# Performance work log

Hardware: AMD Instinct MI355X
Metric: run time of the kernel (lower is better)

Reference implementation:

```python
import jax, jax.numpy as jnp
import numpy as np

D_MODEL = 1024
BLOCK_SIZE = 2048


def setup_inputs() -> dict:
    key = jax.random.key(0)
    ks = jax.random.split(key, 9)
    B, T, C = 4, 2048, D_MODEL
    s = 1.0 / np.sqrt(C)
    return {
        "x": jax.random.normal(ks[0], (B, T, C), dtype=jnp.float32),
        "Wq": jax.random.normal(ks[1], (C, C), dtype=jnp.float32) * s,
        "bq": jnp.zeros((C,), dtype=jnp.float32),
        "Wk": jax.random.normal(ks[2], (C, C), dtype=jnp.float32) * s,
        "bk": jnp.zeros((C,), dtype=jnp.float32),
        "Wv": jax.random.normal(ks[3], (C, C), dtype=jnp.float32) * s,
        "bv": jnp.zeros((C,), dtype=jnp.float32),
        "Wo": jax.random.normal(ks[4], (C, C), dtype=jnp.float32) * s,
        "bo": jnp.zeros((C,), dtype=jnp.float32),
    }


def reference(x, Wq, bq, Wk, bk, Wv, bv, Wo, bo):
    B, T, C = x.shape
    q = x @ Wq + bq
    k = x @ Wk + bk
    v = x @ Wv + bv
    # NOTE: original module never splits heads; attention is over full d_model
    score = jnp.einsum("btc,bsc->bts", q, k) / jnp.sqrt(jnp.asarray(C, x.dtype))
    causal = jnp.tril(jnp.ones((T, T), dtype=bool))
    score = jnp.where(causal, score, jnp.asarray(-jnp.inf, x.dtype))
    probs = jax.nn.softmax(score, axis=-1)
    out = jnp.einsum("bts,bsc->btc", probs, v)
    return out @ Wo + bo
```

## Files before the change

### kernel.cpp

```cpp
#include <hip/hip_runtime.h>
#include <hip/hip_bf16.h>
#include <stdint.h>


typedef __attribute__((ext_vector_type(8))) __bf16 bf16x8;
typedef __attribute__((ext_vector_type(4))) float f32x4;

#define MFMA16(A, B, C) __builtin_amdgcn_mfma_f32_16x16x32_bf16(A, B, C, 0, 0, 0)
#define BAR() asm volatile("s_barrier" ::: "memory")

#define T_SEQ 2048
#define D_MOD 1024

static __device__ __forceinline__ void gload_lds16(const void* g, void* l) {
  __builtin_amdgcn_global_load_lds(
      (const __attribute__((address_space(1))) void*)g,
      (__attribute__((address_space(3))) void*)l, 16, 0, 0);
}

__global__ void cvt_bf16_kernel(const float* __restrict__ in,
                                __bf16* __restrict__ out, int n8) {
  int i = blockIdx.x * blockDim.x + threadIdx.x;
  if (i < n8) {
    const float4* p = (const float4*)(in + (size_t)i * 8);
    float4 a = p[0], b = p[1];
    bf16x8 o;
    o[0] = (__bf16)a.x; o[1] = (__bf16)a.y; o[2] = (__bf16)a.z; o[3] = (__bf16)a.w;
    o[4] = (__bf16)b.x; o[5] = (__bf16)b.y; o[6] = (__bf16)b.z; o[7] = (__bf16)b.w;
    *(bf16x8*)(out + (size_t)i * 8) = o;
  }
}

__global__ void transpose_cvt_kernel(const float* __restrict__ W,
                                     __bf16* __restrict__ Wt) {
  __shared__ float tile[32][33];
  int tx = threadIdx.x, ty = threadIdx.y;
  int bx = blockIdx.x * 32, by = blockIdx.y * 32;
#pragma unroll
  for (int i = 0; i < 4; i++)
    tile[ty + 8 * i][tx] = W[(size_t)(by + ty + 8 * i) * D_MOD + bx + tx];
  __syncthreads();
#pragma unroll
  for (int i = 0; i < 4; i++)
    Wt[(size_t)(bx + ty + 8 * i) * D_MOD + by + tx] = (__bf16)tile[tx][ty + 8 * i];
}

__global__ void transpose_v_kernel(const __bf16* __restrict__ V,
                                   __bf16* __restrict__ Vt) {
  __shared__ __bf16 tile[32][33];
  int tx = threadIdx.x, ty = threadIdx.y;
  int b = blockIdx.z;
  int t0 = blockIdx.x * 32, d0 = blockIdx.y * 32;
  const __bf16* Vb = V + (size_t)b * T_SEQ * D_MOD;
  __bf16* Vtb = Vt + (size_t)b * D_MOD * T_SEQ;
#pragma unroll
  for (int i = 0; i < 4; i++)
    tile[ty + 8 * i][tx] = Vb[(size_t)(t0 + ty + 8 * i) * D_MOD + d0 + tx];
  __syncthreads();
#pragma unroll
  for (int i = 0; i < 4; i++)
    Vtb[(size_t)(d0 + ty + 8 * i) * T_SEQ + t0 + tx] = tile[tx][ty + 8 * i];
}

template <int MG, int NG>
static __device__ __forceinline__ void mfma_quad(f32x4 (&acc)[8][4],
                                                 const bf16x8 (&aR)[4][2],
                                                 const bf16x8 (&bR)[2][2]) {
#pragma unroll
  for (int i = 0; i < 4; i++)
#pragma unroll
    for (int n = 0; n < 2; n++)
#pragma unroll
      for (int kk = 0; kk < 2; kk++)
        acc[MG * 4 + i][NG * 2 + n] =
            MFMA16(aR[i][kk], bR[n][kk], acc[MG * 4 + i][NG * 2 + n]);
}

template <int MODE>
__global__ __launch_bounds__(512, 2) void gemm8_kernel(
    const __bf16* __restrict__ A, const __bf16* __restrict__ Bt,
    const float* __restrict__ b0, const float* __restrict__ b1,
    const float* __restrict__ b2, void* __restrict__ o0,
    void* __restrict__ o1, void* __restrict__ o2, int lda, int ldb,
    size_t bsA, size_t bsB, size_t bsC) {
  constexpr int NT = 16;
  __shared__ __align__(16) char lds[131072];
#define ABUF(p, h) (lds + ((p) * 2 + (h)) * 16384)
#define BBUF(p, h) (lds + 65536 + ((p) * 2 + (h)) * 16384)

  const int tid = threadIdx.x;
  const int w = tid >> 6, l = tid & 63;
  const int wr = w >> 2, wc = w & 3;
  int bm, bn;
  if (MODE == 0) {
    const int cpx = gridDim.x >> 3;
    const int swz = ((int)blockIdx.x & 7) * cpx + ((int)blockIdx.x >> 3);
    bm = (swz / 12) * 256;
    bn = (swz % 12) * 256;
  } else {
    if ((int)blockIdx.y > (int)blockIdx.x) return;
    bm = blockIdx.x * 256;
    bn = blockIdx.y * 256;
  }
  const int z = blockIdx.z;
  A += (size_t)z * bsA;
  Bt += (size_t)z * bsB;

  const int grow = l >> 2;
  const int cswz = (l & 3) ^ ((l >> 3) & 3);
  const int rlo = l & 15;
  const int xsw = (((l >> 4) ^ ((l >> 1) & 3)) << 4);

#define STAGE_A(t, h)                                                        \
  {                                                                          \
    const __bf16* g = A + (size_t)(bm + (h) * 128 + w * 16 + grow) * lda +   \
                      (t) * 64 + cswz * 8;                                   \
    char* d = ABUF((t) & 1, h) + w * 1024 + l * 16;                          \
    gload_lds16(g, d);                                                       \
    gload_lds16(g + 32, d + 8192);                                           \
  }
#define STAGE_B(t, h)                                                        \
  {                                                                          \
    const __bf16* g = Bt + (size_t)(bn + (h) * 128 + w * 16 + grow) * ldb +  \
                      (t) * 64 + cswz * 8;                                   \
    char* d = BBUF((t) & 1, h) + w * 1024 + l * 16;                          \
    gload_lds16(g, d);                                                       \
    gload_lds16(g + 32, d + 8192);                                           \
  }
#define LDA_FRAG(p, g, i, kk)                                     \
  (*(const bf16x8*)(ABUF(p, wr) + (kk) * 8192 +                   \
                    ((g) * 64 + (i) * 16 + rlo) * 64 + xsw))
#define LDB_FRAG(p, g, n, kk)                                     \
  (*(const bf16x8*)(BBUF(p, (wc >> 1)) + (kk) * 8192 +            \
                    ((wc & 1) * 64 + (g) * 32 + (n) * 16 + rlo) * 64 + xsw))

  f32x4 acc[8][4] = {};
  STAGE_A(0, 0); STAGE_A(0, 1);
  STAGE_B(0, 0); STAGE_B(0, 1);
  STAGE_A(1, 0); STAGE_A(1, 1);
  asm volatile("s_waitcnt vmcnt(4)" ::: "memory");
  BAR();

  for (int t = 0; t < NT; ++t) {
    const int p = t & 1;
    bf16x8 a[4][2], b[2][2];
#pragma unroll
    for (int i = 0; i < 4; i++) {
      a[i][0] = LDA_FRAG(p, 0, i, 0);
      a[i][1] = LDA_FRAG(p, 0, i, 1);
    }
#pragma unroll
    for (int n = 0; n < 2; n++) {
      b[n][0] = LDB_FRAG(p, 0, n, 0);
      b[n][1] = LDB_FRAG(p, 0, n, 1);
    }
    if (t + 1 < NT) STAGE_B(t + 1, 0);
    BAR();
    __builtin_amdgcn_s_setprio(1);
    mfma_quad<0, 0>(acc, a, b);
    __builtin_amdgcn_s_setprio(0);
    BAR();
    bf16x8 b2[2][2];
#pragma unroll
    for (int n = 0; n < 2; n++) {
      b2[n][0] = LDB_FRAG(p, 1, n, 0);
      b2[n][1] = LDB_FRAG(p, 1, n, 1);
    }
    if (t + 1 < NT) STAGE_B(t + 1, 1);
    BAR();
    __builtin_amdgcn_s_setprio(1);
    mfma_quad<0, 1>(acc, a, b2);
    __builtin_amdgcn_s_setprio(0);
    BAR();
#pragma unroll
    for (int i = 0; i < 4; i++) {
      a[i][0] = LDA_FRAG(p, 1, i, 0);
      a[i][1] = LDA_FRAG(p, 1, i, 1);
    }
    BAR();
    __builtin_amdgcn_s_setprio(1);
    mfma_quad<1, 1>(acc, a, b2);
    __builtin_amdgcn_s_setprio(0);
    BAR();
#pragma unroll
    for (int n = 0; n < 2; n++) {
      b[n][0] = LDB_FRAG(p, 0, n, 0);
      b[n][1] = LDB_FRAG(p, 0, n, 1);
    }
    if (t + 2 < NT) {
      STAGE_A(t + 2, 0); STAGE_A(t + 2, 1);
      BAR();
      __builtin_amdgcn_s_setprio(1);
      mfma_quad<1, 0>(acc, a, b);
      __builtin_amdgcn_s_setprio(0);
      asm volatile("s_waitcnt vmcnt(4)" ::: "memory");
      BAR();
    } else {
      BAR();
      __builtin_amdgcn_s_setprio(1);
      mfma_quad<1, 0>(acc, a, b);
      __builtin_amdgcn_s_setprio(0);
      asm volatile("s_waitcnt vmcnt(0)" ::: "memory");
      BAR();
    }
  }

  if (MODE == 0) {
    const int seg = bn >> 10;
    const float* bs = (seg == 0) ? b0 : (seg == 1) ? b1 : b2;
    __bf16* os = (__bf16*)((seg == 0) ? o0 : (seg == 1) ? o1 : o2);
    const int bnl = bn & 1023;
#pragma unroll
    for (int n4 = 0; n4 < 4; n4++) {
      int col = bnl + wc * 64 + n4 * 16 + rlo;
      float bvv = bs[col];
#pragma unroll
      for (int mi = 0; mi < 8; mi++) {
        int row = bm + wr * 128 + mi * 16 + (l >> 4) * 4;
#pragma unroll
        for (int r = 0; r < 4; r++)
          os[(size_t)(row + r) * D_MOD + col] = (__bf16)(acc[mi][n4][r] + bvv);
      }
    }
  } else {
    float* os = (float*)o0 + (size_t)z * bsC;
#pragma unroll
    for (int n4 = 0; n4 < 4; n4++) {
      int col = bn + wc * 64 + n4 * 16 + rlo;
#pragma unroll
      for (int mi = 0; mi < 8; mi++) {
        int rowb = bm + wr * 128 + mi * 16 + (l >> 4) * 4;
#pragma unroll
        for (int r = 0; r < 4; r++) {
          int row = rowb + r;
          float v = acc[mi][n4][r] * 0.03125f;
          if (col > row) v = -1e30f;
          os[(size_t)row * T_SEQ + col] = v;
        }
      }
    }
  }
#undef ABUF
#undef BBUF
#undef STAGE_A
#undef STAGE_B
#undef LDA_FRAG
#undef LDB_FRAG
}

template <int MODE>
__global__ __launch_bounds__(512, 2) void ugemm_kernel(
    const __bf16* __restrict__ A, const __bf16* __restrict__ Bt,
    const float* __restrict__ b0, void* __restrict__ o0, int lda, int ldb,
    size_t bsA, size_t bsB, size_t bsC) {
  __shared__ __align__(16) char lds[147456];
#define ABUF(p3) (lds + (p3) * 16384)
#define BBUF(p3) (lds + 49152 + (p3) * 32768)

  const int tid = threadIdx.x;
  const int w = tid >> 6, l = tid & 63;
  const int wr = w >> 2, wc = w & 3;
  const int z = blockIdx.z;

  int bm, bn, NT;
  if (MODE == 1) {
    const int cpx = gridDim.x >> 3;
    const int swz = ((int)blockIdx.x & 7) * cpx + ((int)blockIdx.x >> 3);
    bm = (swz >> 2) * 128; bn = (swz & 3) * 256; NT = 16;
  } else {
    const int i = (int)blockIdx.x >> 2;
    bm = i * 128; bn = ((int)blockIdx.x & 3) * 256; NT = (i + 1) * 2;
  }
  A += (size_t)z * bsA;
  Bt += (size_t)z * bsB;

  const int grow = w * 16 + (l >> 2);
  const int cswz = (l & 3) ^ ((l >> 3) & 3);
  const int rlo = l & 15;
  const int xsw = (((l >> 4) ^ ((l >> 1) & 3)) << 4);

#define STAGE_A(t, p3)                                                       \
  {                                                                          \
    const __bf16* g = A + (size_t)(bm + grow) * lda + (t) * 64 + cswz * 8;   \
    char* d = ABUF(p3) + w * 1024 + l * 16;                                  \
    gload_lds16(g, d);                                                       \
    gload_lds16(g + 32, d + 8192);                                           \
  }
#define STAGE_B(t, p3)                                                       \
  {                                                                          \
    const __bf16* g = Bt + (size_t)(bn + grow) * ldb + (t) * 64 + cswz * 8;  \
    char* d = BBUF(p3) + w * 1024 + l * 16;                                  \
    gload_lds16(g, d);                                                       \
    gload_lds16(g + 32, d + 16384);                                          \
    const __bf16* g2 = g + (size_t)128 * ldb;                                \
    gload_lds16(g2, d + 8192);                                               \
    gload_lds16(g2 + 32, d + 8192 + 16384);                                  \
  }
#define LDA_FRAG(p3, i, kk)                                       \
  (*(const bf16x8*)(ABUF(p3) + (kk) * 8192 +                      \
                    (wr * 64 + (i) * 16 + rlo) * 64 + xsw))
#define LDB_FRAG(p3, n, kk)                                       \
  (*(const bf16x8*)(BBUF(p3) + (kk) * 16384 +                     \
                    (wc * 64 + (n) * 16 + rlo) * 64 + xsw))

  f32x4 acc[4][4] = {};
  STAGE_A(0, 0); STAGE_B(0, 0);
  STAGE_A(1, 1); STAGE_B(1, 1);
  asm volatile("s_waitcnt vmcnt(6)" ::: "memory");
  BAR();

  int p = 0, pn2 = 2;
  for (int t = 0; t < NT; ++t) {
    bf16x8 af[4][2], bf01[2][2], bf23[2][2];
#pragma unroll
    for (int i = 0; i < 4; i++) {
      af[i][0] = LDA_FRAG(p, i, 0);
      af[i][1] = LDA_FRAG(p, i, 1);
    }
#pragma unroll
    for (int n = 0; n < 2; n++) {
      bf01[n][0] = LDB_FRAG(p, n, 0);
      bf01[n][1] = LDB_FRAG(p, n, 1);
    }
    if (t + 2 < NT) STAGE_A(t + 2, pn2);
    BAR();
    __builtin_amdgcn_s_setprio(1);
#pragma unroll
    for (int i = 0; i < 4; i++)
#pragma unroll
      for (int n = 0; n < 2; n++) {
        acc[i][n] = MFMA16(af[i][0], bf01[n][0], acc[i][n]);
        acc[i][n] = MFMA16(af[i][1], bf01[n][1], acc[i][n]);
      }
    __builtin_amdgcn_s_setprio(0);
    BAR();
#pragma unroll
    for (int n = 0; n < 2; n++) {
      bf23[n][0] = LDB_FRAG(p, n + 2, 0);
      bf23[n][1] = LDB_FRAG(p, n + 2, 1);
    }
    if (t + 2 < NT) STAGE_B(t + 2, pn2);
    BAR();
    __builtin_amdgcn_s_setprio(1);
#pragma unroll
    for (int i = 0; i < 4; i++)
#pragma unroll
      for (int n = 0; n < 2; n++) {
        acc[i][n + 2] = MFMA16(af[i][0], bf23[n][0], acc[i][n + 2]);
        acc[i][n + 2] = MFMA16(af[i][1], bf23[n][1], acc[i][n + 2]);
      }
    __builtin_amdgcn_s_setprio(0);
    if (t + 2 < NT) {
      asm volatile("s_waitcnt vmcnt(6)" ::: "memory");
    } else {
      asm volatile("s_waitcnt vmcnt(0)" ::: "memory");
    }
    BAR();
    p = (p + 1 == 3) ? 0 : p + 1;
    pn2 = (pn2 + 1 == 3) ? 0 : pn2 + 1;
  }

  if (MODE == 1) {
    float* os = (float*)o0;
#pragma unroll
    for (int n = 0; n < 4; n++) {
      int col = bn + wc * 64 + n * 16 + rlo;
      float bvv = b0[col];
#pragma unroll
      for (int m = 0; m < 4; m++) {
        int rowb = bm + wr * 64 + m * 16 + (l >> 4) * 4;
#pragma unroll
        for (int r = 0; r < 4; r++)
          os[(size_t)(rowb + r) * D_MOD + col] = acc[m][n][r] + bvv;
      }
    }
  } else {
    __bf16* os = (__bf16*)o0 + (size_t)z * bsC;
#pragma unroll
    for (int n = 0; n < 4; n++) {
      int col = bn + wc * 64 + n * 16 + rlo;
#pragma unroll
      for (int m = 0; m < 4; m++) {
        int rowb = bm + wr * 64 + m * 16 + (l >> 4) * 4;
#pragma unroll
        for (int r = 0; r < 4; r++)
          os[(size_t)(rowb + r) * D_MOD + col] = (__bf16)acc[m][n][r];
      }
    }
  }
#undef ABUF
#undef BBUF
#undef STAGE_A
#undef STAGE_B
#undef LDA_FRAG
#undef LDB_FRAG
}

__global__ __launch_bounds__(256) void softmax_kernel(float* __restrict__ S,
                                                      size_t bstride) {
  const int t = blockIdx.x, b = blockIdx.y;
  float* Srow = S + (size_t)b * bstride + (size_t)t * T_SEQ;
  __bf16* Prow = (__bf16*)Srow;
  const int L = ((t + 1) + 127) & ~127;
  const int tid = threadIdx.x;
  const int base = tid * 8;
  const bool act = base < L;
  float v[8];
  float m = -1e30f;
  if (act) {
    float4 a = *(const float4*)(Srow + base);
    float4 c = *(const float4*)(Srow + base + 4);
    v[0] = a.x; v[1] = a.y; v[2] = a.z; v[3] = a.w;
    v[4] = c.x; v[5] = c.y; v[6] = c.z; v[7] = c.w;
#pragma unroll
    for (int j = 0; j < 8; j++) m = fmaxf(m, v[j]);
  }
#pragma unroll
  for (int off = 1; off < 64; off <<= 1) m = fmaxf(m, __shfl_xor(m, off));
  __shared__ float redm[4], reds[4];
  const int wave = tid >> 6, lane = tid & 63;
  if (lane == 0) redm[wave] = m;
  __syncthreads();
  m = fmaxf(fmaxf(redm[0], redm[1]), fmaxf(redm[2], redm[3]));
  float p[8];
  float s = 0.f;
  if (act) {
#pragma unroll
    for (int j = 0; j < 8; j++) {
      p[j] = __expf(v[j] - m);
      s += p[j];
    }
  }
#pragma unroll
  for (int off = 1; off < 64; off <<= 1) s += __shfl_xor(s, off);
  if (lane == 0) reds[wave] = s;
  __syncthreads();
  const float inv = 1.0f / (reds[0] + reds[1] + reds[2] + reds[3]);
  if (act) {
    bf16x8 o;
#pragma unroll
    for (int j = 0; j < 8; j++) o[j] = (__bf16)(p[j] * inv);
    *(bf16x8*)(Prow + base) = o;
  }
}

extern "C" void kernel_launch(void* const* d_in, const int* in_sizes, int n_in,
                              void* d_out, int out_size, void* d_ws,
                              size_t ws_size, hipStream_t stream) {
  const float* x = (const float*)d_in[0];
  const float* Wq = (const float*)d_in[1];
  const float* bq = (const float*)d_in[2];
  const float* Wk = (const float*)d_in[3];
  const float* bk = (const float*)d_in[4];
  const float* Wv = (const float*)d_in[5];
  const float* bv = (const float*)d_in[6];
  const float* Wo = (const float*)d_in[7];
  const float* bo = (const float*)d_in[8];

  char* ws = (char*)d_ws;
  const size_t MB = 1u << 20;
  const size_t TC = (size_t)T_SEQ * D_MOD;
  const size_t TT = (size_t)T_SEQ * T_SEQ;
  __bf16* xb    = (__bf16*)(ws);
  __bf16* Wqkvt = (__bf16*)(ws + 16 * MB);
  __bf16* Wot   = (__bf16*)(ws + 22 * MB);
  __bf16* Qb    = (__bf16*)(ws + 24 * MB);
  __bf16* Kb    = (__bf16*)(ws + 40 * MB);
  __bf16* Vb    = (__bf16*)(ws + 56 * MB);
  __bf16* Vtb   = (__bf16*)(ws);

  cvt_bf16_kernel<<<4096, 256, 0, stream>>>(x, xb, 8192 * D_MOD / 8);
  dim3 tb(32, 8);
  transpose_cvt_kernel<<<dim3(32, 32), tb, 0, stream>>>(Wq, Wqkvt);
  transpose_cvt_kernel<<<dim3(32, 32), tb, 0, stream>>>(Wk, Wqkvt + 1024 * 1024);
  transpose_cvt_kernel<<<dim3(32, 32), tb, 0, stream>>>(Wv, Wqkvt + 2048 * 1024);
  transpose_cvt_kernel<<<dim3(32, 32), tb, 0, stream>>>(Wo, Wot);
  gemm8_kernel<0><<<384, 512, 0, stream>>>(xb, Wqkvt, bq, bk, bv, Qb, Kb, Vb,
                                           D_MOD, D_MOD, 0, 0, 0);
  transpose_v_kernel<<<dim3(64, 32, 4), tb, 0, stream>>>(Vb, Vtb);

  const bool batched = ws_size >= 137 * MB;
  if (batched) {
    float* S = (float*)(ws + 72 * MB);
    __bf16* AO = Vb;
    gemm8_kernel<3><<<dim3(8, 8, 4), 512, 0, stream>>>(
        Qb, Kb, nullptr, nullptr, nullptr, S, nullptr, nullptr, D_MOD, D_MOD,
        TC, TC, TT);
    softmax_kernel<<<dim3(T_SEQ, 4), 256, 0, stream>>>(S, TT);
    ugemm_kernel<2><<<dim3(64, 1, 4), 512, 0, stream>>>(
        (const __bf16*)S, Vtb, nullptr, AO, 2 * T_SEQ, T_SEQ, TT * 2,
        (size_t)D_MOD * T_SEQ, TC);
    ugemm_kernel<1><<<256, 512, 0, stream>>>(AO, Wot, bo, d_out, D_MOD, D_MOD,
                                             0, 0, 0);
  } else {
    float* S = (float*)(ws + 56 * MB);
    __bf16* AO = Qb;
    for (int b = 0; b < 4; ++b) {
      gemm8_kernel<3><<<dim3(8, 8, 1), 512, 0, stream>>>(
          Qb + b * TC, Kb + b * TC, nullptr, nullptr, nullptr, S, nullptr,
          nullptr, D_MOD, D_MOD, 0, 0, 0);
      softmax_kernel<<<dim3(T_SEQ, 1), 256, 0, stream>>>(S, 0);
      ugemm_kernel<2><<<dim3(64, 1, 1), 512, 0, stream>>>(
          (const __bf16*)S, Vtb + b * TC, nullptr, AO + b * TC, 2 * T_SEQ,
          T_SEQ, 0, 0, 0);
    }
    ugemm_kernel<1><<<256, 512, 0, stream>>>(AO, Wot, bo, d_out, D_MOD, D_MOD,
                                             0, 0, 0);
  }
}
```

Measured before the change: 197.4 us.

## Fuse V transpose into QKV GEMM epilogue with 128x384 tiles, merge weight transposes

```diff
diff --git a/kernel.cpp b/kernel.cpp
--- a/kernel.cpp
+++ b/kernel.cpp
@@ -4,6 +4,7 @@
 
 
 typedef __attribute__((ext_vector_type(8))) __bf16 bf16x8;
+typedef __attribute__((ext_vector_type(4))) __bf16 bf16x4;
 typedef __attribute__((ext_vector_type(4))) float f32x4;
 
 #define MFMA16(A, B, C) __builtin_amdgcn_mfma_f32_16x16x32_bf16(A, B, C, 0, 0, 0)
@@ -31,9 +32,16 @@
   }
 }
 
-__global__ void transpose_cvt_kernel(const float* __restrict__ W,
-                                     __bf16* __restrict__ Wt) {
+__global__ void transpose_cvt4_kernel(const float* __restrict__ Wq,
+                                      const float* __restrict__ Wk,
+                                      const float* __restrict__ Wv,
+                                      const float* __restrict__ Wo,
+                                      __bf16* __restrict__ Wqkvt,
+                                      __bf16* __restrict__ Wot) {
   __shared__ float tile[32][33];
+  const int z = blockIdx.z;
+  const float* W = (z == 0) ? Wq : (z == 1) ? Wk : (z == 2) ? Wv : Wo;
+  __bf16* Wt = (z < 3) ? (Wqkvt + (size_t)z * 1024 * 1024) : Wot;
   int tx = threadIdx.x, ty = threadIdx.y;
   int bx = blockIdx.x * 32, by = blockIdx.y * 32;
 #pragma unroll
@@ -45,21 +53,166 @@
     Wt[(size_t)(bx + ty + 8 * i) * D_MOD + by + tx] = (__bf16)tile[tx][ty + 8 * i];
 }
 
-__global__ void transpose_v_kernel(const __bf16* __restrict__ V,
-                                   __bf16* __restrict__ Vt) {
-  __shared__ __bf16 tile[32][33];
-  int tx = threadIdx.x, ty = threadIdx.y;
-  int b = blockIdx.z;
-  int t0 = blockIdx.x * 32, d0 = blockIdx.y * 32;
-  const __bf16* Vb = V + (size_t)b * T_SEQ * D_MOD;
-  __bf16* Vtb = Vt + (size_t)b * D_MOD * T_SEQ;
-#pragma unroll
-  for (int i = 0; i < 4; i++)
-    tile[ty + 8 * i][tx] = Vb[(size_t)(t0 + ty + 8 * i) * D_MOD + d0 + tx];
-  __syncthreads();
-#pragma unroll
-  for (int i = 0; i < 4; i++)
-    Vtb[(size_t)(d0 + ty + 8 * i) * T_SEQ + t0 + tx] = tile[tx][ty + 8 * i];
+__global__ __launch_bounds__(512, 2) void qkv384_kernel(
+    const __bf16* __restrict__ A, const __bf16* __restrict__ Bt,
+    const float* __restrict__ bq, const float* __restrict__ bk,
+    const float* __restrict__ bv, __bf16* __restrict__ Qo,
+    __bf16* __restrict__ Ko, __bf16* __restrict__ Vto) {
+  constexpr int NT = 16;
+  __shared__ __align__(16) char lds[131072];
+#define ABUF(p) (lds + (p) * 16384)
+#define BBUF(p) (lds + 32768 + (p) * 49152)
+
+  const int tid = threadIdx.x;
+  const int w = tid >> 6, l = tid & 63;
+  const int wr = w >> 2, wc = w & 3;
+  const int cpx = gridDim.x >> 3;
+  const int swz = ((int)blockIdx.x & 7) * cpx + ((int)blockIdx.x >> 3);
+  const int bm = (swz >> 3) * 128;
+  const int bn = (swz & 7) * 384;
+
+  const int cswz = (l & 3) ^ ((l >> 3) & 3);
+  const int rlo = l & 15;
+  const int xsw = (((l >> 4) ^ ((l >> 1) & 3)) << 4);
+
+#define STAGE_A(t, p)                                                     \
+  {                                                                       \
+    const __bf16* g = A + (size_t)(bm + w * 16 + (l >> 2)) * 1024 +       \
+                      (t) * 64 + cswz * 8;                                \
+    char* d = ABUF(p) + w * 1024 + l * 16;                                \
+    gload_lds16(g, d);                                                    \
+    gload_lds16(g + 32, d + 8192);                                        \
+  }
+#define STAGE_B(t, p, gch)                                                \
+  {                                                                       \
+    const __bf16* g = Bt +                                                \
+        (size_t)(bn + ((gch) * 8 + w) * 16 + (l >> 2)) * 1024 +           \
+        (t) * 64 + cswz * 8;                                              \
+    char* d = BBUF(p) + ((gch) * 8 + w) * 1024 + l * 16;                  \
+    gload_lds16(g, d);                                                    \
+    gload_lds16(g + 32, d + 24576);                                       \
+  }
+#define LDA_FRAG(p, i, kk)                                        \
+  (*(const bf16x8*)(ABUF(p) + (kk) * 8192 +                       \
+                    (wr * 64 + (i) * 16 + rlo) * 64 + xsw))
+#define LDB_FRAG(p, gch, n, kk)                                   \
+  (*(const bf16x8*)(BBUF(p) + (kk) * 24576 +                      \
+                    (wc * 96 + (gch) * 32 + (n) * 16 + rlo) * 64 + xsw))
+
+  f32x4 acc[4][6] = {};
+  STAGE_A(0, 0);
+  STAGE_B(0, 0, 0); STAGE_B(0, 0, 1); STAGE_B(0, 0, 2);
+  STAGE_A(1, 1);
+  asm volatile("s_waitcnt vmcnt(2)" ::: "memory");
+  BAR();
+
+  for (int t = 0; t < NT; ++t) {
+    const int p = t & 1;
+    bf16x8 a[4][2], bfr[2][2];
+#pragma unroll
+    for (int i = 0; i < 4; i++) {
+      a[i][0] = LDA_FRAG(p, i, 0);
+      a[i][1] = LDA_FRAG(p, i, 1);
+    }
+#pragma unroll
+    for (int n = 0; n < 2; n++) {
+      bfr[n][0] = LDB_FRAG(p, 0, n, 0);
+      bfr[n][1] = LDB_FRAG(p, 0, n, 1);
+    }
+    if (t + 1 < NT) {
+      STAGE_B(t + 1, p ^ 1, 0);
+      STAGE_B(t + 1, p ^ 1, 1);
+      STAGE_B(t + 1, p ^ 1, 2);
+    }
+    BAR();
+    __builtin_amdgcn_s_setprio(1);
+#pragma unroll
+    for (int i = 0; i < 4; i++)
+#pragma unroll
+      for (int n = 0; n < 2; n++) {
+        acc[i][n] = MFMA16(a[i][0], bfr[n][0], acc[i][n]);
+        acc[i][n] = MFMA16(a[i][1], bfr[n][1], acc[i][n]);
+      }
+    __builtin_amdgcn_s_setprio(0);
+    BAR();
+#pragma unroll
+    for (int n = 0; n < 2; n++) {
+      bfr[n][0] = LDB_FRAG(p, 1, n, 0);
+      bfr[n][1] = LDB_FRAG(p, 1, n, 1);
+    }
+    if (t + 2 < NT) STAGE_A(t + 2, p);
+    BAR();
+    __builtin_amdgcn_s_setprio(1);
+#pragma unroll
+    for (int i = 0; i < 4; i++)
+#pragma unroll
+      for (int n = 0; n < 2; n++) {
+        acc[i][2 + n] = MFMA16(a[i][0], bfr[n][0], acc[i][2 + n]);
+        acc[i][2 + n] = MFMA16(a[i][1], bfr[n][1], acc[i][2 + n]);
+      }
+    __builtin_amdgcn_s_setprio(0);
+    BAR();
+#pragma unroll
+    for (int n = 0; n < 2; n++) {
+      bfr[n][0] = LDB_FRAG(p, 2, n, 0);
+      bfr[n][1] = LDB_FRAG(p, 2, n, 1);
+    }
+    BAR();
+    __builtin_amdgcn_s_setprio(1);
+#pragma unroll
+    for (int i = 0; i < 4; i++)
+#pragma unroll
+      for (int n = 0; n < 2; n++) {
+        acc[i][4 + n] = MFMA16(a[i][0], bfr[n][0], acc[i][4 + n]);
+        acc[i][4 + n] = MFMA16(a[i][1], bfr[n][1], acc[i][4 + n]);
+      }
+    __builtin_amdgcn_s_setprio(0);
+    if (t < NT - 2) asm volatile("s_waitcnt vmcnt(2)" ::: "memory");
+    else asm volatile("s_waitcnt vmcnt(0)" ::: "memory");
+    BAR();
+  }
+
+  const int l4 = (l >> 4) * 4;
+#pragma unroll
+  for (int gch = 0; gch < 3; gch++)
+#pragma unroll
+    for (int n = 0; n < 2; n++) {
+      const int cbase = bn + wc * 96 + gch * 32 + n * 16;
+      const int seg = cbase >> 10;
+      const int lcol = (cbase & 1023) + rlo;
+      const int an = gch * 2 + n;
+      if (seg < 2) {
+        const float* bs = seg ? bk : bq;
+        __bf16* os = seg ? Ko : Qo;
+        const float bvv = bs[lcol];
+#pragma unroll
+        for (int i = 0; i < 4; i++) {
+          const int rowb = bm + wr * 64 + i * 16 + l4;
+#pragma unroll
+          for (int r = 0; r < 4; r++)
+            os[(size_t)(rowb + r) * D_MOD + lcol] =
+                (__bf16)(acc[i][an][r] + bvv);
+        }
+      } else {
+        const float bvv = bv[lcol];
+#pragma unroll
+        for (int i = 0; i < 4; i++) {
+          const int rowb = bm + wr * 64 + i * 16 + l4;
+          const int z = rowb >> 11, tt = rowb & 2047;
+          bf16x4 pk;
+#pragma unroll
+          for (int r = 0; r < 4; r++) pk[r] = (__bf16)(acc[i][an][r] + bvv);
+          *(bf16x4*)(Vto + (size_t)z * (D_MOD * T_SEQ) +
+                     (size_t)lcol * T_SEQ + tt) = pk;
+        }
+      }
+    }
+#undef ABUF
+#undef BBUF
+#undef STAGE_A
+#undef STAGE_B
+#undef LDA_FRAG
+#undef LDB_FRAG
 }
 
 template <int MG, int NG>
@@ -76,13 +229,9 @@
             MFMA16(aR[i][kk], bR[n][kk], acc[MG * 4 + i][NG * 2 + n]);
 }
 
-template <int MODE>
-__global__ __launch_bounds__(512, 2) void gemm8_kernel(
+__global__ __launch_bounds__(512, 2) void qk_kernel(
     const __bf16* __restrict__ A, const __bf16* __restrict__ Bt,
-    const float* __restrict__ b0, const float* __restrict__ b1,
-    const float* __restrict__ b2, void* __restrict__ o0,
-    void* __restrict__ o1, void* __restrict__ o2, int lda, int ldb,
-    size_t bsA, size_t bsB, size_t bsC) {
+    float* __restrict__ So, size_t bsA, size_t bsB, size_t bsC) {
   constexpr int NT = 16;
   __shared__ __align__(16) char lds[131072];
 #define ABUF(p, h) (lds + ((p) * 2 + (h)) * 16384)
@@ -91,17 +240,8 @@
   const int tid = threadIdx.x;
   const int w = tid >> 6, l = tid & 63;
   const int wr = w >> 2, wc = w & 3;
-  int bm, bn;
-  if (MODE == 0) {
-    const int cpx = gridDim.x >> 3;
-    const int swz = ((int)blockIdx.x & 7) * cpx + ((int)blockIdx.x >> 3);
-    bm = (swz / 12) * 256;
-    bn = (swz % 12) * 256;
-  } else {
-    if ((int)blockIdx.y > (int)blockIdx.x) return;
-    bm = blockIdx.x * 256;
-    bn = blockIdx.y * 256;
-  }
+  if ((int)blockIdx.y > (int)blockIdx.x) return;
+  const int bm = blockIdx.x * 256, bn = blockIdx.y * 256;
   const int z = blockIdx.z;
   A += (size_t)z * bsA;
   Bt += (size_t)z * bsB;
@@ -111,21 +251,21 @@
   const int rlo = l & 15;
   const int xsw = (((l >> 4) ^ ((l >> 1) & 3)) << 4);
 
-#define STAGE_A(t, h)                                                        \
-  {                                                                          \
-    const __bf16* g = A + (size_t)(bm + (h) * 128 + w * 16 + grow) * lda +   \
-                      (t) * 64 + cswz * 8;                                   \
-    char* d = ABUF((t) & 1, h) + w * 1024 + l * 16;                          \
-    gload_lds16(g, d);                                                       \
-    gload_lds16(g + 32, d + 8192);                                           \
-  }
-#define STAGE_B(t, h)                                                        \
-  {                                                                          \
-    const __bf16* g = Bt + (size_t)(bn + (h) * 128 + w * 16 + grow) * ldb +  \
-                      (t) * 64 + cswz * 8;                                   \
-    char* d = BBUF((t) & 1, h) + w * 1024 + l * 16;                          \
-    gload_lds16(g, d);                                                       \
-    gload_lds16(g + 32, d + 8192);                                           \
+#define STAGE_A(t, h)                                                       \
+  {                                                                         \
+    const __bf16* g = A + (size_t)(bm + (h) * 128 + w * 16 + grow) * 1024 + \
+                      (t) * 64 + cswz * 8;                                  \
+    char* d = ABUF((t) & 1, h) + w * 1024 + l * 16;                         \
+    gload_lds16(g, d);                                                      \
+    gload_lds16(g + 32, d + 8192);                                          \
+  }
+#define STAGE_B(t, h)                                                       \
+  {                                                                         \
+    const __bf16* g = Bt + (size_t)(bn + (h) * 128 + w * 16 + grow) * 1024 +\
+                      (t) * 64 + cswz * 8;                                  \
+    char* d = BBUF((t) & 1, h) + w * 1024 + l * 16;                         \
+    gload_lds16(g, d);                                                      \
+    gload_lds16(g + 32, d + 8192);                                          \
   }
 #define LDA_FRAG(p, g, i, kk)                                     \
   (*(const bf16x8*)(ABUF(p, wr) + (kk) * 8192 +                   \
@@ -205,38 +345,19 @@
     }
   }
 
-  if (MODE == 0) {
-    const int seg = bn >> 10;
-    const float* bs = (seg == 0) ? b0 : (seg == 1) ? b1 : b2;
-    __bf16* os = (__bf16*)((seg == 0) ? o0 : (seg == 1) ? o1 : o2);
-    const int bnl = bn & 1023;
-#pragma unroll
-    for (int n4 = 0; n4 < 4; n4++) {
-      int col = bnl + wc * 64 + n4 * 16 + rlo;
-      float bvv = bs[col];
-#pragma unroll
-      for (int mi = 0; mi < 8; mi++) {
-        int row = bm + wr * 128 + mi * 16 + (l >> 4) * 4;
-#pragma unroll
-        for (int r = 0; r < 4; r++)
-          os[(size_t)(row + r) * D_MOD + col] = (__bf16)(acc[mi][n4][r] + bvv);
-      }
-    }
-  } else {
-    float* os = (float*)o0 + (size_t)z * bsC;
-#pragma unroll
-    for (int n4 = 0; n4 < 4; n4++) {
-      int col = bn + wc * 64 + n4 * 16 + rlo;
-#pragma unroll
-      for (int mi = 0; mi < 8; mi++) {
-        int rowb = bm + wr * 128 + mi * 16 + (l >> 4) * 4;
-#pragma unroll
-        for (int r = 0; r < 4; r++) {
-          int row = rowb + r;
-          float v = acc[mi][n4][r] * 0.03125f;
-          if (col > row) v = -1e30f;
-          os[(size_t)row * T_SEQ + col] = v;
-        }
+  float* os = So + (size_t)z * bsC;
+#pragma unroll
+  for (int n4 = 0; n4 < 4; n4++) {
+    int col = bn + wc * 64 + n4 * 16 + rlo;
+#pragma unroll
+    for (int mi = 0; mi < 8; mi++) {
+      int rowb = bm + wr * 128 + mi * 16 + (l >> 4) * 4;
+#pragma unroll
+      for (int r = 0; r < 4; r++) {
+        int row = rowb + r;
+        float v = acc[mi][n4][r] * 0.03125f;
+        if (col > row) v = -1e30f;
+        os[(size_t)row * T_SEQ + col] = v;
       }
     }
   }
@@ -466,39 +587,29 @@
   __bf16* Wot   = (__bf16*)(ws + 22 * MB);
   __bf16* Qb    = (__bf16*)(ws + 24 * MB);
   __bf16* Kb    = (__bf16*)(ws + 40 * MB);
-  __bf16* Vb    = (__bf16*)(ws + 56 * MB);
-  __bf16* Vtb   = (__bf16*)(ws);
+  __bf16* Vtb   = (__bf16*)(ws + 56 * MB);
 
   cvt_bf16_kernel<<<4096, 256, 0, stream>>>(x, xb, 8192 * D_MOD / 8);
-  dim3 tb(32, 8);
-  transpose_cvt_kernel<<<dim3(32, 32), tb, 0, stream>>>(Wq, Wqkvt);
-  transpose_cvt_kernel<<<dim3(32, 32), tb, 0, stream>>>(Wk, Wqkvt + 1024 * 1024);
-  transpose_cvt_kernel<<<dim3(32, 32), tb, 0, stream>>>(Wv, Wqkvt + 2048 * 1024);
-  transpose_cvt_kernel<<<dim3(32, 32), tb, 0, stream>>>(Wo, Wot);
-  gemm8_kernel<0><<<384, 512, 0, stream>>>(xb, Wqkvt, bq, bk, bv, Qb, Kb, Vb,
-                                           D_MOD, D_MOD, 0, 0, 0);
-  transpose_v_kernel<<<dim3(64, 32, 4), tb, 0, stream>>>(Vb, Vtb);
+  transpose_cvt4_kernel<<<dim3(32, 32, 4), dim3(32, 8), 0, stream>>>(
+      Wq, Wk, Wv, Wo, Wqkvt, Wot);
+  qkv384_kernel<<<512, 512, 0, stream>>>(xb, Wqkvt, bq, bk, bv, Qb, Kb, Vtb);
 
   const bool batched = ws_size >= 137 * MB;
   if (batched) {
     float* S = (float*)(ws + 72 * MB);
-    __bf16* AO = Vb;
-    gemm8_kernel<3><<<dim3(8, 8, 4), 512, 0, stream>>>(
-        Qb, Kb, nullptr, nullptr, nullptr, S, nullptr, nullptr, D_MOD, D_MOD,
-        TC, TC, TT);
+    __bf16* AO = Qb;
+    qk_kernel<<<dim3(8, 8, 4), 512, 0, stream>>>(Qb, Kb, S, TC, TC, TT);
     softmax_kernel<<<dim3(T_SEQ, 4), 256, 0, stream>>>(S, TT);
     ugemm_kernel<2><<<dim3(64, 1, 4), 512, 0, stream>>>(
-        (const __bf16*)S, Vtb, nullptr, AO, 2 * T_SEQ, T_SEQ, TT * 2,
-        (size_t)D_MOD * T_SEQ, TC);
+        (const __bf16*)S, Vtb, nullptr, AO, 2 * T_SEQ, T_SEQ, TT * 2, TC, TC);
     ugemm_kernel<1><<<256, 512, 0, stream>>>(AO, Wot, bo, d_out, D_MOD, D_MOD,
                                              0, 0, 0);
   } else {
-    float* S = (float*)(ws + 56 * MB);
+    float* S = (float*)(ws);
     __bf16* AO = Qb;
     for (int b = 0; b < 4; ++b) {
-      gemm8_kernel<3><<<dim3(8, 8, 1), 512, 0, stream>>>(
-          Qb + b * TC, Kb + b * TC, nullptr, nullptr, nullptr, S, nullptr,
-          nullptr, D_MOD, D_MOD, 0, 0, 0);
+      qk_kernel<<<dim3(8, 8, 1), 512, 0, stream>>>(Qb + b * TC, Kb + b * TC, S,
+                                                   0, 0, 0);
       softmax_kernel<<<dim3(T_SEQ, 1), 256, 0, stream>>>(S, 0);
       ugemm_kernel<2><<<dim3(64, 1, 1), 512, 0, stream>>>(
           (const __bf16*)S, Vtb + b * TC, nullptr, AO + b * TC, 2 * T_SEQ,
```

Result: faster. 185.5 us (-6.0%).
